# Optimization experiments

Measured on AMD Instinct MI355X. Metric: run time of the kernel, lower is better.

The kernel has to match this reference:

```python
import jax, jax.numpy as jnp
import numpy as np

E, D, H, K = 8, 768, 3072, 2   # num_experts, embed_size, expert_size, top-k
TAU = 1.0
BN, PN = 32, 196

def l2norm(v):
    # F.normalize(p=2, dim=-1), eps=1e-12
    return v / jnp.maximum(jnp.linalg.norm(v, axis=-1, keepdims=True), 1e-12)

def setup_inputs() -> dict:
    key = jax.random.key(0)
    ks = jax.random.split(key, 8)
    s = 0.02  # weight init scale for stability
    return {
        "x": jax.random.normal(ks[0], (BN, PN, D), dtype=jnp.float32),
        "Wlinear": jax.random.normal(ks[1], (D, D), dtype=jnp.float32) * s,
        "learnedE": jax.random.normal(ks[2], (E, D), dtype=jnp.float32),
        "bias": jnp.zeros((BN * PN, E), dtype=jnp.float32),
        "W1": jax.random.normal(ks[3], (E, D, H), dtype=jnp.float32) * s,
        "b1": jnp.zeros((E, H), dtype=jnp.float32),
        "W2": jax.random.normal(ks[4], (E, H, D), dtype=jnp.float32) * s,
        "b2": jnp.zeros((E, D), dtype=jnp.float32),
        "sW1": jax.random.normal(ks[5], (D, H), dtype=jnp.float32) * s,
        "sb1": jnp.zeros((H,), dtype=jnp.float32),
        "sW2": jax.random.normal(ks[6], (H, D), dtype=jnp.float32) * s,
        "sb2": jnp.zeros((D,), dtype=jnp.float32),
    }

def reference(x, Wlinear, learnedE, bias, W1, b1, W2, b2, sW1, sb1, sW2, sb2):
    bn, pn, d = x.shape
    patches = x.reshape(bn * pn, d)                      # [T, D]
    proj = l2norm(patches @ Wlinear.T)                   # router projection
    routed = proj @ l2norm(learnedE).T                   # [T, E] cosine scores
    probs = jax.nn.softmax((routed + bias) / TAU, axis=1)  # eval path (no noise)
    k_probs, k_idx = jax.lax.top_k(probs, K)             # [T, K]
    # combine weights: scatter top-k probs into dense [T, E] gate matrix
    T = probs.shape[0]
    gates = jnp.zeros_like(probs).at[jnp.arange(T)[:, None], k_idx].add(k_probs)
    # expert MLPs computed densely for all experts, masked by gates
    h = jax.nn.gelu(jnp.einsum('td,edh->teh', patches, W1) + b1[None], approximate=False)
    eo = jnp.einsum('teh,ehd->ted', h, W2) + b2[None]    # [T, E, D]
    moe = jnp.einsum('ted,te->td', eo, gates)            # weighted combine
    # shared expert (expert_list[-1]) applied to every token; dropout is identity in eval
    shared = jax.nn.gelu(patches @ sW1 + sb1, approximate=False) @ sW2 + sb2
    return (moe + shared).reshape(bn, pn, d)
```

## Files before the change

### kernel.cpp

```cpp
#include <hip/hip_runtime.h>
#include <hip/hip_bf16.h>

typedef __hip_bfloat16 bf16;
typedef __attribute__((ext_vector_type(8))) short short8;
typedef __attribute__((ext_vector_type(4))) float f32x4;

#define T_TOK 6272
#define D_DIM 768
#define H_DIM 3072
#define NEXP 8
#define MAXTILES 160
#define BKR 64

#define S_BARRIER() __builtin_amdgcn_s_barrier()
#define WAIT_VM0() asm volatile("s_waitcnt vmcnt(0)" ::: "memory")

__device__ __forceinline__ void async16(void* lds, const void* g) {
  __builtin_amdgcn_global_load_lds(
      (const __attribute__((address_space(1))) void*)g,
      (__attribute__((address_space(3))) void*)lds, 16, 0, 0);
}

__device__ __forceinline__ float gelu_f(float x) {
  float z = x * 0.70710678118654752f;
  float az = fabsf(z);
  float t = 1.f / (1.f + 0.3275911f * az);
  float poly = ((((1.061405429f * t - 1.453152027f) * t + 1.421413741f) * t -
                 0.284496736f) * t + 0.254829592f) * t;
  float e = __expf(-az * az);
  float er = 1.f - poly * e;
  er = copysignf(er, z);
  return 0.5f * x * (1.f + er);
}

__device__ __forceinline__ int xcd_work(int orig, int nwr) {
  if (orig >= nwr) return -1;
  int xcd = orig & 7, pos = orig >> 3;
  int q = nwr >> 3, r = nwr & 7;
  return (xcd < r ? xcd * (q + 1) : r * (q + 1) + (xcd - r) * q) + pos;
}


__global__ void cast_hilo(const float* __restrict__ in, bf16* __restrict__ hi,
                          bf16* __restrict__ lo, int n) {
  int i = blockIdx.x * blockDim.x + threadIdx.x;
  int stride = gridDim.x * blockDim.x;
  for (; i < n; i += stride) {
    float x = in[i];
    bf16 h = __float2bfloat16(x);
    hi[i] = h;
    lo[i] = __float2bfloat16(x - __bfloat162float(h));
  }
}

__global__ void transpose_cast(const float* __restrict__ in, bf16* __restrict__ out,
                               int R, int C) {
  __shared__ float tile[32][33];
  int b = blockIdx.z;
  const float* ib = in + (size_t)b * R * C;
  bf16* ob = out + (size_t)b * R * C;
  int r0 = blockIdx.x * 32, c0 = blockIdx.y * 32;
  int tx = threadIdx.x & 31, ty = threadIdx.x >> 5;
  for (int i = 0; i < 32; i += 8)
    tile[ty + i][tx] = ib[(size_t)(r0 + ty + i) * C + c0 + tx];
  __syncthreads();
  for (int i = 0; i < 32; i += 8)
    ob[(size_t)(c0 + ty + i) * R + r0 + tx] = __float2bfloat16(tile[tx][ty + i]);
}

__global__ void norm_learnedE(const float* __restrict__ lE, float* __restrict__ eHat) {
  int wave = threadIdx.x >> 6, lane = threadIdx.x & 63;
  for (int e = wave; e < NEXP; e += 4) {
    float v[12];
    float ss = 0.f;
    for (int j = 0; j < 12; j++) {
      v[j] = lE[e * D_DIM + lane + 64 * j];
      ss += v[j] * v[j];
    }
    for (int o = 32; o; o >>= 1) ss += __shfl_xor(ss, o);
    float rn = 1.f / fmaxf(sqrtf(ss), 1e-12f);
    for (int j = 0; j < 12; j++) eHat[e * D_DIM + lane + 64 * j] = v[j] * rn;
  }
}


__global__ __launch_bounds__(256, 2) void gemm_router(
    const bf16* __restrict__ pHi, const bf16* __restrict__ pLo,
    const bf16* __restrict__ wHi, const bf16* __restrict__ wLo,
    float* __restrict__ y) {
  int work = xcd_work(blockIdx.x, 294);
  int tileG = work / 48;
  int rem = work - tileG * 48;
  int base = tileG * 8;
  int gl = 49 - base; if (gl > 8) gl = 8;
  int colb = rem / gl;
  int rowt = base + rem % gl;

  __shared__ __align__(16) bf16 As[2][128 * BKR];
  __shared__ __align__(16) bf16 Bs[2][128 * BKR];
  int tid = threadIdx.x, wave = tid >> 6, lane = tid & 63;
  int wr = wave >> 1, wc = wave & 1;
  int rowbase = rowt * 128, colbase = colb * 128;
  int rslot = (lane & 7) ^ (lane >> 3);

  size_t aoff[4], boff[4];
#pragma unroll
  for (int c = 0; c < 4; c++) {
    int row = 32 * wave + 8 * c + (lane >> 3);
    aoff[c] = (size_t)(rowbase + row) * D_DIM + rslot * 8;
    boff[c] = (size_t)(colbase + row) * D_DIM + rslot * 8;
  }

  auto stage = [&](int buf, int ks) {
    int term = ks / 12;
    const bf16* A = (term == 1) ? pLo : pHi;
    const bf16* B = (term == 2) ? wLo : wHi;
    int kk = (ks - term * 12) * BKR;
#pragma unroll
    for (int c = 0; c < 4; c++) {
      async16(&As[buf][(32 * wave + 8 * c) * BKR], A + aoff[c] + kk);
      async16(&Bs[buf][(32 * wave + 8 * c) * BKR], B + boff[c] + kk);
    }
  };

  f32x4 acc[4][4];
#pragma unroll
  for (int m = 0; m < 4; m++)
#pragma unroll
    for (int n = 0; n < 4; n++) acc[m][n] = 0.f;

  stage(0, 0);
  __syncthreads();
  int cur = 0;
  int q = lane >> 4, fr = lane & 15;
  for (int ks = 0; ks < 36; ks++) {
    if (ks < 35) stage(cur ^ 1, ks + 1);
    const bf16* Ac = As[cur];
    const bf16* Bc = Bs[cur];
#pragma unroll
    for (int kh = 0; kh < 2; kh++) {
      short8 af[4], bfr[4];
#pragma unroll
      for (int m = 0; m < 4; m++) {
        int row = wr * 64 + m * 16 + fr;
        int ls = ((kh << 2) + q) ^ (row & 7);
        af[m] = *(const short8*)&Ac[row * BKR + ls * 8];
      }
#pragma unroll
      for (int n = 0; n < 4; n++) {
        int row = wc * 64 + n * 16 + fr;
        int ls = ((kh << 2) + q) ^ (row & 7);
        bfr[n] = *(const short8*)&Bc[row * BKR + ls * 8];
      }
#pragma unroll
      for (int m = 0; m < 4; m++)
#pragma unroll
        for (int n = 0; n < 4; n++)
          acc[m][n] = __builtin_amdgcn_mfma_f32_16x16x32_bf16(af[m], bfr[n], acc[m][n], 0, 0, 0);
    }
    __syncthreads();
    cur ^= 1;
  }
  for (int m = 0; m < 4; m++)
    for (int n = 0; n < 4; n++)
      for (int j = 0; j < 4; j++) {
        int r = rowbase + wr * 64 + m * 16 + (lane >> 4) * 4 + j;
        int c = colbase + wc * 64 + n * 16 + (lane & 15);
        y[(size_t)r * D_DIM + c] = acc[m][n][j];
      }
}


__global__ void router_epi(const float* __restrict__ y, const float* __restrict__ eHat,
                           const float* __restrict__ bias, int* __restrict__ gidx,
                           float* __restrict__ gval, int* __restrict__ counts) {
  int wave = threadIdx.x >> 6, lane = threadIdx.x & 63;
  int t = blockIdx.x * 4 + wave;
  float v[12];
  float ss = 0.f;
  for (int j = 0; j < 12; j++) {
    v[j] = y[(size_t)t * D_DIM + lane + 64 * j];
    ss += v[j] * v[j];
  }
  for (int o = 32; o; o >>= 1) ss += __shfl_xor(ss, o);
  float d[NEXP];
  for (int e = 0; e < NEXP; e++) {
    float s = 0.f;
    for (int j = 0; j < 12; j++) s += v[j] * eHat[e * D_DIM + lane + 64 * j];
    for (int o = 32; o; o >>= 1) s += __shfl_xor(s, o);
    d[e] = s;
  }
  if (lane == 0) {
    float rn = 1.f / fmaxf(sqrtf(ss), 1e-12f);
    float sc[NEXP], mx = -1e30f;
    for (int e = 0; e < NEXP; e++) {
      sc[e] = d[e] * rn + bias[t * NEXP + e];
      mx = fmaxf(mx, sc[e]);
    }
    float p[NEXP], sum = 0.f;
    for (int e = 0; e < NEXP; e++) {
      p[e] = expf(sc[e] - mx);
      sum += p[e];
    }
    float inv = 1.f / sum;
    int i1 = 0;
    for (int e = 1; e < NEXP; e++)
      if (sc[e] > sc[i1]) i1 = e;
    int i2 = -1;
    for (int e = 0; e < NEXP; e++) {
      if (e == i1) continue;
      if (i2 < 0 || sc[e] > sc[i2]) i2 = e;
    }
    gidx[t * 2] = i1;
    gidx[t * 2 + 1] = i2;
    gval[t * 2] = p[i1] * inv;
    gval[t * 2 + 1] = p[i2] * inv;
    atomicAdd(&counts[i1], 1);
    atomicAdd(&counts[i2], 1);
  }
}


__global__ void scan_build(const int* __restrict__ counts, int* __restrict__ segstart,
                           int* __restrict__ cursors, int* __restrict__ tiles,
                           int* __restrict__ numtiles) {
  if (threadIdx.x == 0) {
    int off = 0;
    for (int e = 0; e < NEXP; e++) {
      segstart[e] = off;
      cursors[e] = off;
      off += counts[e];
    }
    segstart[NEXP] = off;
    segstart[NEXP + 1] = off + T_TOK;
    int nt = 0;
    for (int e = 0; e < NEXP + 1; e++) {
      int cnt = (e < NEXP) ? counts[e] : T_TOK;
      int ntl = (cnt + 127) >> 7;
      for (int l = 0; l < ntl; l++) {
        tiles[nt * 2] = e;
        tiles[nt * 2 + 1] = l;
        nt++;
      }
    }
    *numtiles = nt;
  }
}

__global__ void fill_assign(const int* __restrict__ gidx, int* __restrict__ cursors,
                            int* __restrict__ rowtok, int* __restrict__ slot_of) {
  int t = blockIdx.x * 256 + threadIdx.x;
  if (t >= T_TOK) return;
  for (int k = 0; k < 2; k++) {
    int e = gidx[t * 2 + k];
    int pos = atomicAdd(&cursors[e], 1);
    rowtok[pos] = t;
    slot_of[t * 2 + k] = pos;
  }
  rowtok[2 * T_TOK + t] = t;
}



__global__ __launch_bounds__(256, 4) void gemm_ffn1(
    const bf16* __restrict__ pHi, const bf16* __restrict__ W1T,
    const bf16* __restrict__ sW1T, const float* __restrict__ b1,
    const float* __restrict__ sb1, const int* __restrict__ segstart,
    const int* __restrict__ tiles, const int* __restrict__ numtiles,
    const int* __restrict__ rowtok, bf16* __restrict__ hbuf) {
  const int NC = 24, G = 16;
  int nt = *numtiles;
  int work = xcd_work(blockIdx.x + NC * blockIdx.y, nt * NC);
  if (work < 0) return;
  int tileG = work / (NC * G);
  int rem = work - tileG * (NC * G);
  int tbase = tileG * G;
  int gl = nt - tbase; if (gl > G) gl = G;
  int colb = rem / gl;
  int gx = tbase + rem % gl;

  int seg = tiles[gx * 2], lt = tiles[gx * 2 + 1];
  int s0 = segstart[seg] + lt * 128;
  int send = segstart[seg + 1];
  const bf16* Bw = (seg < NEXP) ? W1T + (size_t)seg * H_DIM * D_DIM : sW1T;
  const float* bb = (seg < NEXP) ? b1 + seg * H_DIM : sb1;

  __shared__ __align__(16) bf16 As[2][128 * 32];
  __shared__ __align__(16) bf16 Bs[2][128 * 32];
  int tid = threadIdx.x, wave = tid >> 6, lane = tid & 63;
  int wr = wave >> 1, wc = wave & 1;
  int colbase = colb * 128;
  int q = lane >> 4, fr = lane & 15;
  int g8 = (((lane & 3) ^ ((lane >> 3) & 3))) * 8;
  int ls8 = (q ^ ((fr >> 1) & 3)) * 8;

  const bf16* aptr[2];
  const bf16* bptr[2];
#pragma unroll
  for (int p = 0; p < 2; p++) {
    int r = wave * 32 + p * 16 + (lane >> 2);
    int s = s0 + r;
    if (s > send - 1) s = send - 1;
    aptr[p] = pHi + (size_t)rowtok[s] * D_DIM + g8;
    bptr[p] = Bw + (size_t)(colbase + r) * D_DIM + g8;
  }

  auto stage = [&](int buf, int ks) {
    int kk = ks * 32;
#pragma unroll
    for (int p = 0; p < 2; p++) {
      async16(&As[buf][(wave * 32 + p * 16) * 32], aptr[p] + kk);
      async16(&Bs[buf][(wave * 32 + p * 16) * 32], bptr[p] + kk);
    }
  };

  f32x4 acc[4][4];
#pragma unroll
  for (int m = 0; m < 4; m++)
#pragma unroll
    for (int n = 0; n < 4; n++) acc[m][n] = 0.f;

  stage(0, 0);
  WAIT_VM0();
  S_BARRIER();

#define NT1 24
  for (int ks = 0; ks < NT1; ks++) {
    if (ks + 1 < NT1) stage((ks + 1) & 1, ks + 1);
    const bf16* Ac = As[ks & 1];
    const bf16* Bc = Bs[ks & 1];
    short8 af[4], bfr[4];
#pragma unroll
    for (int m = 0; m < 4; m++)
      af[m] = *(const short8*)&Ac[(wr * 64 + m * 16 + fr) * 32 + ls8];
#pragma unroll
    for (int n = 0; n < 4; n++)
      bfr[n] = *(const short8*)&Bc[(wc * 64 + n * 16 + fr) * 32 + ls8];
    __builtin_amdgcn_s_setprio(1);
#pragma unroll
    for (int m = 0; m < 4; m++)
#pragma unroll
      for (int n = 0; n < 4; n++)
        acc[m][n] = __builtin_amdgcn_mfma_f32_16x16x32_bf16(af[m], bfr[n], acc[m][n], 0, 0, 0);
    __builtin_amdgcn_s_setprio(0);
    WAIT_VM0();
    S_BARRIER();
  }
#pragma unroll
  for (int n = 0; n < 4; n++) {
    int c = colbase + wc * 64 + n * 16 + fr;
    float bv = bb[c];
#pragma unroll
    for (int m = 0; m < 4; m++)
#pragma unroll
      for (int j = 0; j < 4; j++) {
        int s = s0 + wr * 64 + m * 16 + q * 4 + j;
        if (s < send) {
          float xv = acc[m][n][j] + bv;
          hbuf[(size_t)s * H_DIM + c] = __float2bfloat16(gelu_f(xv));
        }
      }
  }
}


__global__ __launch_bounds__(256, 4) void gemm_ffn2(
    const bf16* __restrict__ hbuf, const bf16* __restrict__ W2T,
    const bf16* __restrict__ sW2T, const float* __restrict__ b2,
    const float* __restrict__ sb2, const int* __restrict__ segstart,
    const int* __restrict__ tiles, const int* __restrict__ numtiles,
    float* __restrict__ moebuf) {
  const int NC = 6, G = 4;
  int nt = *numtiles;
  int work = xcd_work(blockIdx.x + NC * blockIdx.y, nt * NC);
  if (work < 0) return;
  int tileG = work / (NC * G);
  int rem = work - tileG * (NC * G);
  int tbase = tileG * G;
  int gl = nt - tbase; if (gl > G) gl = G;
  int colb = rem / gl;
  int gx = tbase + rem % gl;

  int seg = tiles[gx * 2], lt = tiles[gx * 2 + 1];
  int s0 = segstart[seg] + lt * 128;
  int send = segstart[seg + 1];
  const bf16* Bw = (seg < NEXP) ? W2T + (size_t)seg * H_DIM * D_DIM : sW2T;
  const float* bb = (seg < NEXP) ? b2 + seg * D_DIM : sb2;

  __shared__ __align__(16) bf16 As[2][128 * 32];
  __shared__ __align__(16) bf16 Bs[2][128 * 32];
  int tid = threadIdx.x, wave = tid >> 6, lane = tid & 63;
  int wr = wave >> 1, wc = wave & 1;
  int colbase = colb * 128;
  int q = lane >> 4, fr = lane & 15;
  int g8 = (((lane & 3) ^ ((lane >> 3) & 3))) * 8;
  int ls8 = (q ^ ((fr >> 1) & 3)) * 8;

  const bf16* aptr[2];
  const bf16* bptr[2];
#pragma unroll
  for (int p = 0; p < 2; p++) {
    int r = wave * 32 + p * 16 + (lane >> 2);
    int s = s0 + r;
    if (s > send - 1) s = send - 1;
    aptr[p] = hbuf + (size_t)s * H_DIM + g8;
    bptr[p] = Bw + (size_t)(colbase + r) * H_DIM + g8;
  }

  auto stage = [&](int buf, int ks) {
    int kk = ks * 32;
#pragma unroll
    for (int p = 0; p < 2; p++) {
      async16(&As[buf][(wave * 32 + p * 16) * 32], aptr[p] + kk);
      async16(&Bs[buf][(wave * 32 + p * 16) * 32], bptr[p] + kk);
    }
  };

  f32x4 acc[4][4];
#pragma unroll
  for (int m = 0; m < 4; m++)
#pragma unroll
    for (int n = 0; n < 4; n++) acc[m][n] = 0.f;

  stage(0, 0);
  WAIT_VM0();
  S_BARRIER();

#define NT2 96
  for (int ks = 0; ks < NT2; ks++) {
    if (ks + 1 < NT2) stage((ks + 1) & 1, ks + 1);
    const bf16* Ac = As[ks & 1];
    const bf16* Bc = Bs[ks & 1];
    short8 af[4], bfr[4];
#pragma unroll
    for (int m = 0; m < 4; m++)
      af[m] = *(const short8*)&Ac[(wr * 64 + m * 16 + fr) * 32 + ls8];
#pragma unroll
    for (int n = 0; n < 4; n++)
      bfr[n] = *(const short8*)&Bc[(wc * 64 + n * 16 + fr) * 32 + ls8];
    __builtin_amdgcn_s_setprio(1);
#pragma unroll
    for (int m = 0; m < 4; m++)
#pragma unroll
      for (int n = 0; n < 4; n++)
        acc[m][n] = __builtin_amdgcn_mfma_f32_16x16x32_bf16(af[m], bfr[n], acc[m][n], 0, 0, 0);
    __builtin_amdgcn_s_setprio(0);
    WAIT_VM0();
    S_BARRIER();
  }
#pragma unroll
  for (int n = 0; n < 4; n++) {
    int c = colbase + wc * 64 + n * 16 + fr;
    float bv = bb[c];
#pragma unroll
    for (int m = 0; m < 4; m++)
#pragma unroll
      for (int j = 0; j < 4; j++) {
        int s = s0 + wr * 64 + m * 16 + q * 4 + j;
        if (s < send) moebuf[(size_t)s * D_DIM + c] = acc[m][n][j] + bv;
      }
  }
}


__global__ void combine_out(const float* __restrict__ moebuf, const float* __restrict__ gval,
                            const int* __restrict__ slot_of, float* __restrict__ out) {
  int i = blockIdx.x * 256 + threadIdx.x;
  const int total = T_TOK * (D_DIM / 4);
  if (i >= total) return;
  int t = i / (D_DIM / 4), c = i % (D_DIM / 4);
  float g0 = gval[2 * t], g1 = gval[2 * t + 1];
  int sA = slot_of[2 * t], sB = slot_of[2 * t + 1];
  const f32x4* pa = (const f32x4*)(moebuf + (size_t)sA * D_DIM) + c;
  const f32x4* pb = (const f32x4*)(moebuf + (size_t)sB * D_DIM) + c;
  const f32x4* ps = (const f32x4*)(moebuf + (size_t)(2 * T_TOK + t) * D_DIM) + c;
  f32x4 r = g0 * (*pa) + g1 * (*pb) + *ps;
  ((f32x4*)out)[i] = r;
}


extern "C" void kernel_launch(void* const* d_in, const int* in_sizes, int n_in,
                              void* d_out, int out_size, void* d_ws, size_t ws_size,
                              hipStream_t stream) {
  const float* x = (const float*)d_in[0];
  const float* Wlinear = (const float*)d_in[1];
  const float* learnedE = (const float*)d_in[2];
  const float* bias = (const float*)d_in[3];
  const float* W1 = (const float*)d_in[4];
  const float* b1 = (const float*)d_in[5];
  const float* W2 = (const float*)d_in[6];
  const float* b2 = (const float*)d_in[7];
  const float* sW1 = (const float*)d_in[8];
  const float* sb1 = (const float*)d_in[9];
  const float* sW2 = (const float*)d_in[10];
  const float* sb2 = (const float*)d_in[11];
  float* out = (float*)d_out;

  char* ws = (char*)d_ws;
  size_t off = 0;
  auto alloc = [&](size_t bytes) {
    char* p = ws + off;
    off += (bytes + 255) & ~(size_t)255;
    return p;
  };
  float* eHat = (float*)alloc(8 * 768 * 4);
  bf16* pHi = (bf16*)alloc((size_t)T_TOK * D_DIM * 2);
  bf16* pLo = (bf16*)alloc((size_t)T_TOK * D_DIM * 2);
  bf16* wHi = (bf16*)alloc((size_t)D_DIM * D_DIM * 2);
  bf16* wLo = (bf16*)alloc((size_t)D_DIM * D_DIM * 2);
  bf16* W1T = (bf16*)alloc((size_t)NEXP * D_DIM * H_DIM * 2);
  bf16* W2T = (bf16*)alloc((size_t)NEXP * D_DIM * H_DIM * 2);
  bf16* sW1T = (bf16*)alloc((size_t)D_DIM * H_DIM * 2);
  bf16* sW2T = (bf16*)alloc((size_t)D_DIM * H_DIM * 2);
  float* y = (float*)alloc((size_t)T_TOK * D_DIM * 4);
  bf16* hbuf = (bf16*)alloc((size_t)3 * T_TOK * H_DIM * 2);
  float* moebuf = (float*)alloc((size_t)3 * T_TOK * D_DIM * 4);
  int* gidx = (int*)alloc(T_TOK * 2 * 4);
  float* gval = (float*)alloc(T_TOK * 2 * 4);
  int* rowtok = (int*)alloc(3 * T_TOK * 4);
  int* slot_of = (int*)alloc(T_TOK * 2 * 4);
  int* counts = (int*)alloc(8 * 4);
  int* segstart = (int*)alloc(10 * 4);
  int* cursors = (int*)alloc(8 * 4);
  int* numtiles = (int*)alloc(4);
  int* tiles = (int*)alloc(MAXTILES * 2 * 4);
  (void)ws_size; (void)in_sizes; (void)n_in; (void)out_size;

  hipMemsetAsync(counts, 0, 8 * 4, stream);
  norm_learnedE<<<1, 256, 0, stream>>>(learnedE, eHat);
  cast_hilo<<<2048, 256, 0, stream>>>(x, pHi, pLo, T_TOK * D_DIM);
  cast_hilo<<<1024, 256, 0, stream>>>(Wlinear, wHi, wLo, D_DIM * D_DIM);
  transpose_cast<<<dim3(D_DIM / 32, H_DIM / 32, NEXP), 256, 0, stream>>>(W1, W1T, D_DIM, H_DIM);
  transpose_cast<<<dim3(H_DIM / 32, D_DIM / 32, NEXP), 256, 0, stream>>>(W2, W2T, H_DIM, D_DIM);
  transpose_cast<<<dim3(D_DIM / 32, H_DIM / 32, 1), 256, 0, stream>>>(sW1, sW1T, D_DIM, H_DIM);
  transpose_cast<<<dim3(H_DIM / 32, D_DIM / 32, 1), 256, 0, stream>>>(sW2, sW2T, H_DIM, D_DIM);

  gemm_router<<<294, 256, 0, stream>>>(pHi, pLo, wHi, wLo, y);
  router_epi<<<T_TOK / 4, 256, 0, stream>>>(y, eHat, bias, gidx, gval, counts);
  scan_build<<<1, 64, 0, stream>>>(counts, segstart, cursors, tiles, numtiles);
  fill_assign<<<(T_TOK + 255) / 256, 256, 0, stream>>>(gidx, cursors, rowtok, slot_of);

  gemm_ffn1<<<dim3(24, MAXTILES), 256, 0, stream>>>(
      pHi, W1T, sW1T, b1, sb1, segstart, tiles, numtiles, rowtok, hbuf);
  gemm_ffn2<<<dim3(6, MAXTILES), 256, 0, stream>>>(
      hbuf, W2T, sW2T, b2, sb2, segstart, tiles, numtiles, moebuf);

  combine_out<<<(T_TOK * (D_DIM / 4) + 255) / 256, 256, 0, stream>>>(moebuf, gval, slot_of, out);
}
```

Measured before the change: 671.7 us.

## Fuse gated combine into FFN2 epilogue via atomic adds to output

```diff
diff --git a/kernel.cpp b/kernel.cpp
--- a/kernel.cpp
+++ b/kernel.cpp
@@ -13,6 +13,7 @@
 #define BKR 64
 
 #define S_BARRIER() __builtin_amdgcn_s_barrier()
+#define WAIT_VM4() asm volatile("s_waitcnt vmcnt(4)" ::: "memory")
 #define WAIT_VM0() asm volatile("s_waitcnt vmcnt(0)" ::: "memory")
 
 __device__ __forceinline__ void async16(void* lds, const void* g) {
@@ -247,17 +248,19 @@
   }
 }
 
-__global__ void fill_assign(const int* __restrict__ gidx, int* __restrict__ cursors,
-                            int* __restrict__ rowtok, int* __restrict__ slot_of) {
+__global__ void fill_assign(const int* __restrict__ gidx, const float* __restrict__ gval,
+                            int* __restrict__ cursors, int* __restrict__ rowtok,
+                            float* __restrict__ slotgate) {
   int t = blockIdx.x * 256 + threadIdx.x;
   if (t >= T_TOK) return;
   for (int k = 0; k < 2; k++) {
     int e = gidx[t * 2 + k];
     int pos = atomicAdd(&cursors[e], 1);
     rowtok[pos] = t;
-    slot_of[t * 2 + k] = pos;
+    slotgate[pos] = gval[t * 2 + k];
   }
   rowtok[2 * T_TOK + t] = t;
+  slotgate[2 * T_TOK + t] = 1.0f;
 }
 
 
@@ -369,7 +372,8 @@
     const bf16* __restrict__ sW2T, const float* __restrict__ b2,
     const float* __restrict__ sb2, const int* __restrict__ segstart,
     const int* __restrict__ tiles, const int* __restrict__ numtiles,
-    float* __restrict__ moebuf) {
+    const int* __restrict__ rowtok, const float* __restrict__ slotgate,
+    float* __restrict__ out) {
   const int NC = 6, G = 4;
   int nt = *numtiles;
   int work = xcd_work(blockIdx.x + NC * blockIdx.y, nt * NC);
@@ -448,6 +452,19 @@
     WAIT_VM0();
     S_BARRIER();
   }
+
+  int tk[16];
+  float sg[16];
+#pragma unroll
+  for (int m = 0; m < 4; m++)
+#pragma unroll
+    for (int j = 0; j < 4; j++) {
+      int s = s0 + wr * 64 + m * 16 + q * 4 + j;
+      bool valid = s < send;
+      int sc = valid ? s : send - 1;
+      tk[m * 4 + j] = rowtok[sc];
+      sg[m * 4 + j] = valid ? slotgate[sc] : 0.f;
+    }
 #pragma unroll
   for (int n = 0; n < 4; n++) {
     int c = colbase + wc * 64 + n * 16 + fr;
@@ -456,26 +473,10 @@
     for (int m = 0; m < 4; m++)
 #pragma unroll
       for (int j = 0; j < 4; j++) {
-        int s = s0 + wr * 64 + m * 16 + q * 4 + j;
-        if (s < send) moebuf[(size_t)s * D_DIM + c] = acc[m][n][j] + bv;
+        float v = (acc[m][n][j] + bv) * sg[m * 4 + j];
+        atomicAdd(&out[(size_t)tk[m * 4 + j] * D_DIM + c], v);
       }
   }
-}
-
-
-__global__ void combine_out(const float* __restrict__ moebuf, const float* __restrict__ gval,
-                            const int* __restrict__ slot_of, float* __restrict__ out) {
-  int i = blockIdx.x * 256 + threadIdx.x;
-  const int total = T_TOK * (D_DIM / 4);
-  if (i >= total) return;
-  int t = i / (D_DIM / 4), c = i % (D_DIM / 4);
-  float g0 = gval[2 * t], g1 = gval[2 * t + 1];
-  int sA = slot_of[2 * t], sB = slot_of[2 * t + 1];
-  const f32x4* pa = (const f32x4*)(moebuf + (size_t)sA * D_DIM) + c;
-  const f32x4* pb = (const f32x4*)(moebuf + (size_t)sB * D_DIM) + c;
-  const f32x4* ps = (const f32x4*)(moebuf + (size_t)(2 * T_TOK + t) * D_DIM) + c;
-  f32x4 r = g0 * (*pa) + g1 * (*pb) + *ps;
-  ((f32x4*)out)[i] = r;
 }
 
 
@@ -514,11 +515,10 @@
   bf16* sW2T = (bf16*)alloc((size_t)D_DIM * H_DIM * 2);
   float* y = (float*)alloc((size_t)T_TOK * D_DIM * 4);
   bf16* hbuf = (bf16*)alloc((size_t)3 * T_TOK * H_DIM * 2);
-  float* moebuf = (float*)alloc((size_t)3 * T_TOK * D_DIM * 4);
   int* gidx = (int*)alloc(T_TOK * 2 * 4);
   float* gval = (float*)alloc(T_TOK * 2 * 4);
   int* rowtok = (int*)alloc(3 * T_TOK * 4);
-  int* slot_of = (int*)alloc(T_TOK * 2 * 4);
+  float* slotgate = (float*)alloc(3 * T_TOK * 4);
   int* counts = (int*)alloc(8 * 4);
   int* segstart = (int*)alloc(10 * 4);
   int* cursors = (int*)alloc(8 * 4);
@@ -527,6 +527,7 @@
   (void)ws_size; (void)in_sizes; (void)n_in; (void)out_size;
 
   hipMemsetAsync(counts, 0, 8 * 4, stream);
+  hipMemsetAsync(out, 0, (size_t)T_TOK * D_DIM * 4, stream);
   norm_learnedE<<<1, 256, 0, stream>>>(learnedE, eHat);
   cast_hilo<<<2048, 256, 0, stream>>>(x, pHi, pLo, T_TOK * D_DIM);
   cast_hilo<<<1024, 256, 0, stream>>>(Wlinear, wHi, wLo, D_DIM * D_DIM);
@@ -538,12 +539,10 @@
   gemm_router<<<294, 256, 0, stream>>>(pHi, pLo, wHi, wLo, y);
   router_epi<<<T_TOK / 4, 256, 0, stream>>>(y, eHat, bias, gidx, gval, counts);
   scan_build<<<1, 64, 0, stream>>>(counts, segstart, cursors, tiles, numtiles);
-  fill_assign<<<(T_TOK + 255) / 256, 256, 0, stream>>>(gidx, cursors, rowtok, slot_of);
+  fill_assign<<<(T_TOK + 255) / 256, 256, 0, stream>>>(gidx, gval, cursors, rowtok, slotgate);
 
   gemm_ffn1<<<dim3(24, MAXTILES), 256, 0, stream>>>(
       pHi, W1T, sW1T, b1, sb1, segstart, tiles, numtiles, rowtok, hbuf);
   gemm_ffn2<<<dim3(6, MAXTILES), 256, 0, stream>>>(
-      hbuf, W2T, sW2T, b2, sb2, segstart, tiles, numtiles, moebuf);
-
-  combine_out<<<(T_TOK * (D_DIM / 4) + 255) / 256, 256, 0, stream>>>(moebuf, gval, slot_of, out);
-}
+      hbuf, W2T, sW2T, b2, sb2, segstart, tiles, numtiles, rowtok, slotgate, out);
+}
```

Measured after the change: 696.8 us. 3.7% more time.
